# Kernel tuning notes

Hardware: AMD Instinct MI355X
Metric: run time of the kernel (lower is better)

Reference implementation:

```python
import jax, jax.numpy as jnp
import numpy as np

B, S, D, H = 2, 2048, 1024, 16
DEPTH = D // H


def setup_inputs() -> dict:
    key = jax.random.key(0)
    ks = jax.random.split(key, 9)
    sc = 1.0 / np.sqrt(D)
    return {
        "x": jax.random.normal(ks[0], (B, S, D), dtype=jnp.float32),
        "wq": jax.random.normal(ks[1], (D, D), dtype=jnp.float32) * sc,
        "bq": jnp.zeros((D,), dtype=jnp.float32),
        "wk": jax.random.normal(ks[2], (D, D), dtype=jnp.float32) * sc,
        "bk": jnp.zeros((D,), dtype=jnp.float32),
        "wv": jax.random.normal(ks[3], (D, D), dtype=jnp.float32) * sc,
        "bv": jnp.zeros((D,), dtype=jnp.float32),
        "wo": jax.random.normal(ks[4], (D, D), dtype=jnp.float32) * sc,
        "bo": jnp.zeros((D,), dtype=jnp.float32),
    }


def _split_heads(t):
    # [B,S,D] -> [B,H,S,depth]
    return t.reshape(B, S, H, DEPTH).transpose(0, 2, 1, 3)


def reference(x, wq, bq, wk, bk, wv, bv, wo, bo):
    q = _split_heads(x @ wq + bq)
    k = _split_heads(x @ wk + bk)
    v = _split_heads(x @ wv + bv)
    scale = 1.0 / jnp.sqrt(jnp.asarray(DEPTH, dtype=x.dtype))
    logits = jnp.einsum("bhqd,bhkd->bhqk", q, k) * scale
    attn = jax.nn.relu(logits)  # ReLU replaces softmax
    ctx = jnp.einsum("bhqk,bhkd->bhqd", attn, v)
    concat = ctx.transpose(0, 2, 1, 3).reshape(B, S, D)
    out = concat @ wo + bo
    return out, attn
```

## Files before the change

### kernel.cpp

```cpp
#include <hip/hip_runtime.h>
#include <hip/hip_bf16.h>

constexpr int Bn = 2, Sn = 2048, Dn = 1024, Hn = 16, DEP = 64;
constexpr int NTOKn = Bn * Sn;

typedef __bf16 bf16x8 __attribute__((ext_vector_type(8)));
typedef float f32x4 __attribute__((ext_vector_type(4)));

__device__ __forceinline__ unsigned short f2bf(float f) {
    union { __hip_bfloat16 h; unsigned short u; } cv;
    cv.h = __float2bfloat16(f);
    return cv.u;
}

__device__ __forceinline__ void gll16(const void* g, void* l) {
    __builtin_amdgcn_global_load_lds(
        (const __attribute__((address_space(1))) unsigned int*)g,
        (__attribute__((address_space(3))) unsigned int*)l, 16, 0, 0);
}

__global__ __launch_bounds__(256) void k_cvt_x(const float* __restrict__ x,
                                               unsigned short* __restrict__ xb,
                                               int n) {
    int idx = (blockIdx.x * 256 + threadIdx.x) * 4;
    if (idx < n) {
        float4 v = *reinterpret_cast<const float4*>(x + idx);
        ushort4 o;
        o.x = f2bf(v.x); o.y = f2bf(v.y); o.z = f2bf(v.z); o.w = f2bf(v.w);
        *reinterpret_cast<ushort4*>(xb + idx) = o;
    }
}

__global__ __launch_bounds__(256) void k_tconv_w(const float* __restrict__ w0,
                                                 const float* __restrict__ w1,
                                                 const float* __restrict__ w2,
                                                 const float* __restrict__ w3,
                                                 unsigned short* __restrict__ t0,
                                                 unsigned short* __restrict__ t1,
                                                 unsigned short* __restrict__ t2,
                                                 unsigned short* __restrict__ t3) {
    const float* w; unsigned short* tp;
    switch (blockIdx.z) {
        case 0: w = w0; tp = t0; break;
        case 1: w = w1; tp = t1; break;
        case 2: w = w2; tp = t2; break;
        default: w = w3; tp = t3; break;
    }
    __shared__ unsigned short tile[64][65];
    const int k0 = blockIdx.x * 64, n0 = blockIdx.y * 64;
    const int t = threadIdx.x;
    const int c = t & 63, rb = t >> 6;
#pragma unroll
    for (int i = 0; i < 16; ++i) {
        int r = rb + i * 4;
        tile[r][c] = f2bf(w[(size_t)(k0 + r) * Dn + n0 + c]);
    }
    __syncthreads();
#pragma unroll
    for (int i = 0; i < 16; ++i) {
        int n = rb + i * 4;
        tp[(size_t)(n0 + n) * Dn + k0 + c] = tile[c][n];
    }
}

__global__ __launch_bounds__(256) void k_tr_v(const unsigned short* __restrict__ V,
                                              unsigned short* __restrict__ VT) {
    __shared__ unsigned short tile[64][65];
    const int s0 = blockIdx.x * 64;
    const int bh = blockIdx.y;
    const int b = bh >> 4, h = bh & 15;
    const int t = threadIdx.x;
    const int c = t & 63, rb = t >> 6;
#pragma unroll
    for (int i = 0; i < 16; ++i) {
        int r = rb + i * 4;
        tile[r][c] = V[(size_t)(b * Sn + s0 + r) * Dn + h * DEP + c];
    }
    __syncthreads();
#pragma unroll
    for (int i = 0; i < 16; ++i) {
        int d = rb + i * 4;
        VT[(size_t)(bh * DEP + d) * Sn + s0 + c] = tile[c][d];
    }
}

template <bool OUT_F32, bool QKV3>
__global__ __launch_bounds__(256) void k_gemm(const unsigned short* __restrict__ A,
                                              const unsigned short* __restrict__ Bt_,
                                              const float* __restrict__ b0,
                                              const float* __restrict__ b1,
                                              const float* __restrict__ b2,
                                              void* __restrict__ C_,
                                              int M, int N, int K) {
    __shared__ unsigned short As[128][32];
    __shared__ unsigned short Bs[128][32];
    const int t = threadIdx.x;
    const int w = t >> 6, l = t & 63;
    const int m0 = blockIdx.x * 128, n0 = blockIdx.y * 128;
    const int wr = (w >> 1) * 64, wc = (w & 1) * 64;

    const unsigned short* Bt = Bt_;
    const float* bias = b0;
    char* Cb = (char*)C_;
    if (QKV3) {
        const int z = blockIdx.z;
        Bt = Bt_ + (size_t)z * N * K;
        bias = (z == 0) ? b0 : (z == 1 ? b1 : b2);
        Cb = (char*)C_ + (size_t)z * M * N * (OUT_F32 ? 4 : 2);
    }

    const int lrow = t >> 2;
    const int lcol = (t & 3) * 8;
    const unsigned short* gA = A + (size_t)(m0 + lrow) * K + lcol;
    const unsigned short* gB = Bt + (size_t)(n0 + lrow) * K + lcol;
    unsigned short* lA = &As[0][0] + t * 8;
    unsigned short* lB = &Bs[0][0] + t * 8;

    f32x4 acc[4][4] = {};

    for (int k0 = 0; k0 < K; k0 += 32) {
        __syncthreads();
        gll16(gA + k0, lA);
        gll16(gA + (size_t)64 * K + k0, lA + 2048);
        gll16(gB + k0, lB);
        gll16(gB + (size_t)64 * K + k0, lB + 2048);
        __syncthreads();

        bf16x8 af[4], bfv[4];
#pragma unroll
        for (int i = 0; i < 4; ++i)
            af[i] = *reinterpret_cast<const bf16x8*>(&As[wr + i * 16 + (l & 15)][(l >> 4) * 8]);
#pragma unroll
        for (int i = 0; i < 4; ++i)
            bfv[i] = *reinterpret_cast<const bf16x8*>(&Bs[wc + i * 16 + (l & 15)][(l >> 4) * 8]);
#pragma unroll
        for (int mi = 0; mi < 4; ++mi)
#pragma unroll
            for (int ni = 0; ni < 4; ++ni)
                acc[mi][ni] =
                    __builtin_amdgcn_mfma_f32_16x16x32_bf16(af[mi], bfv[ni], acc[mi][ni], 0, 0, 0);
    }

#pragma unroll
    for (int mi = 0; mi < 4; ++mi) {
        const int row = m0 + wr + mi * 16 + (l >> 4) * 4;
#pragma unroll
        for (int ni = 0; ni < 4; ++ni) {
            const int col = n0 + wc + ni * 16 + (l & 15);
            const float bv = bias[col];
#pragma unroll
            for (int i = 0; i < 4; ++i) {
                const float v = acc[mi][ni][i] + bv;
                if (OUT_F32)
                    reinterpret_cast<float*>(Cb)[(size_t)(row + i) * N + col] = v;
                else
                    reinterpret_cast<unsigned short*>(Cb)[(size_t)(row + i) * N + col] = f2bf(v);
            }
        }
    }
}

__global__ __launch_bounds__(256, 2) void k_attn(const unsigned short* __restrict__ Qb,
                                                 const unsigned short* __restrict__ Kb,
                                                 const unsigned short* __restrict__ VTb,
                                                 float* __restrict__ attn,
                                                 unsigned short* __restrict__ ctx) {
    __shared__ unsigned short Ks[128 * 64];
    __shared__ unsigned short Vs[64 * 128];
    __shared__ unsigned short Ps[4][32][136];

    const int t = threadIdx.x;
    const int w = t >> 6, l = t & 63;
    const int q0 = blockIdx.x * 128;
    const int bh = blockIdx.y;
    const int b = bh >> 4, h = bh & 15;
    const float scale = 0.125f;

    bf16x8 qf[2][2];
#pragma unroll
    for (int mi = 0; mi < 2; ++mi)
#pragma unroll
        for (int kk = 0; kk < 2; ++kk)
            qf[mi][kk] = *reinterpret_cast<const bf16x8*>(
                Qb + (size_t)(b * Sn + q0 + w * 32 + mi * 16 + (l & 15)) * Dn + h * DEP +
                kk * 32 + (l >> 4) * 8);

    const int krow = t >> 3;
    const int kcolswz = ((t & 7) * 8) ^ ((krow & 7) << 3);
    const int vrow = t >> 4;
    const int vcolswz = ((t & 15) * 8) ^ ((vrow & 7) << 3);
    unsigned short* lK = Ks + t * 8;
    unsigned short* lV = Vs + t * 8;

    f32x4 ctxa[2][4] = {};
    f32x4 sa[2][8];

    float* const abase = attn + (size_t)bh * Sn * Sn + (size_t)(q0 + w * 32) * Sn;

    auto STAGE = [&](int kb) {
#pragma unroll
        for (int is = 0; is < 4; ++is) {
            gll16(Kb + (size_t)(b * Sn + kb * 128 + is * 32 + krow) * Dn + h * DEP + kcolswz,
                  lK + is * 2048);
            gll16(VTb + (size_t)(bh * DEP + is * 16 + vrow) * Sn + kb * 128 + vcolswz,
                  lV + is * 2048);
        }
    };

    auto QKT = [&]() {
#pragma unroll
        for (int mi = 0; mi < 2; ++mi)
#pragma unroll
            for (int nj = 0; nj < 8; ++nj)
                sa[mi][nj] = (f32x4){0.f, 0.f, 0.f, 0.f};
#pragma unroll
        for (int nj = 0; nj < 8; ++nj) {
            const int kr = nj * 16 + (l & 15);
#pragma unroll
            for (int kk = 0; kk < 2; ++kk) {
                const int kidx = (kr * 64 + kk * 32 + (l >> 4) * 8) ^ ((kr & 7) << 3);
                const bf16x8 bfr = *reinterpret_cast<const bf16x8*>(Ks + kidx);
                sa[0][nj] = __builtin_amdgcn_mfma_f32_16x16x32_bf16(qf[0][kk], bfr, sa[0][nj], 0, 0, 0);
                sa[1][nj] = __builtin_amdgcn_mfma_f32_16x16x32_bf16(qf[1][kk], bfr, sa[1][nj], 0, 0, 0);
            }
        }
#pragma unroll
        for (int mi = 0; mi < 2; ++mi) {
#pragma unroll
            for (int nj = 0; nj < 8; ++nj) {
                f32x4 v = sa[mi][nj];
#pragma unroll
                for (int i = 0; i < 4; ++i) {
                    float p = v[i] * scale;
                    v[i] = p > 0.f ? p : 0.f;
                }
                sa[mi][nj] = v;
                const int kc = nj * 16 + (l & 15);
#pragma unroll
                for (int i = 0; i < 4; ++i)
                    Ps[w][mi * 16 + (l >> 4) * 4 + i][kc] = f2bf(v[i]);
            }
        }
    };

    auto PV = [&]() {
        bf16x8 pf[2][4];
#pragma unroll
        for (int mi = 0; mi < 2; ++mi)
#pragma unroll
            for (int kk = 0; kk < 4; ++kk)
                pf[mi][kk] = *reinterpret_cast<const bf16x8*>(
                    &Ps[w][mi * 16 + (l & 15)][kk * 32 + (l >> 4) * 8]);
#pragma unroll
        for (int nd = 0; nd < 4; ++nd) {
            const int vr = nd * 16 + (l & 15);
#pragma unroll
            for (int kk = 0; kk < 4; ++kk) {
                const int vidx = (vr * 128 + kk * 32 + (l >> 4) * 8) ^ ((vr & 7) << 3);
                const bf16x8 vfr = *reinterpret_cast<const bf16x8*>(Vs + vidx);
                ctxa[0][nd] = __builtin_amdgcn_mfma_f32_16x16x32_bf16(pf[0][kk], vfr, ctxa[0][nd], 0, 0, 0);
                ctxa[1][nd] = __builtin_amdgcn_mfma_f32_16x16x32_bf16(pf[1][kk], vfr, ctxa[1][nd], 0, 0, 0);
            }
        }
    };

    auto STORE_SA = [&](int kb) {
        float* arow = abase + kb * 128;
#pragma unroll
        for (int mi = 0; mi < 2; ++mi)
#pragma unroll
            for (int nj = 0; nj < 8; ++nj) {
                const int kc = nj * 16 + (l & 15);
#pragma unroll
                for (int i = 0; i < 4; ++i)
                    arow[(size_t)(mi * 16 + (l >> 4) * 4 + i) * Sn + kc] = sa[mi][nj][i];
            }
    };

    STAGE(0);
    asm volatile("s_waitcnt vmcnt(0)" ::: "memory");
    __builtin_amdgcn_s_barrier();
    __builtin_amdgcn_sched_barrier(0);
    QKT();
    PV();

    for (int kb = 1; kb < Sn / 128; ++kb) {
        asm volatile("s_waitcnt lgkmcnt(0)" ::: "memory");
        __builtin_amdgcn_s_barrier();
        __builtin_amdgcn_sched_barrier(0);
        STAGE(kb);
        asm volatile("" ::: "memory");
        STORE_SA(kb - 1);
        asm volatile("s_waitcnt vmcnt(63)" ::: "memory");
        __builtin_amdgcn_s_barrier();
        __builtin_amdgcn_sched_barrier(0);
        QKT();
        PV();
    }
    STORE_SA(Sn / 128 - 1);

#pragma unroll
    for (int mi = 0; mi < 2; ++mi) {
#pragma unroll
        for (int nd = 0; nd < 4; ++nd) {
            const int dc = nd * 16 + (l & 15);
#pragma unroll
            for (int i = 0; i < 4; ++i) {
                const int qr = q0 + w * 32 + mi * 16 + (l >> 4) * 4 + i;
                ctx[(size_t)(b * Sn + qr) * Dn + h * DEP + dc] = f2bf(ctxa[mi][nd][i]);
            }
        }
    }
}

extern "C" void kernel_launch(void* const* d_in, const int* in_sizes, int n_in,
                              void* d_out, int out_size, void* d_ws, size_t ws_size,
                              hipStream_t stream) {
    (void)in_sizes; (void)n_in; (void)out_size; (void)ws_size;
    const float* x  = (const float*)d_in[0];
    const float* wq = (const float*)d_in[1];
    const float* bq = (const float*)d_in[2];
    const float* wk = (const float*)d_in[3];
    const float* bk = (const float*)d_in[4];
    const float* wv = (const float*)d_in[5];
    const float* bv = (const float*)d_in[6];
    const float* wo = (const float*)d_in[7];
    const float* bo = (const float*)d_in[8];

    float* out  = (float*)d_out;
    float* attn = out + (size_t)Bn * Sn * Dn;

    char* ws = (char*)d_ws;
    unsigned short* xb = (unsigned short*)ws;  ws += (size_t)NTOKn * Dn * 2;
    unsigned short* wT = (unsigned short*)ws;  ws += (size_t)4 * Dn * Dn * 2;
    unsigned short* qkv = (unsigned short*)ws; ws += (size_t)3 * NTOKn * Dn * 2;
    unsigned short* vT = (unsigned short*)ws;  ws += (size_t)NTOKn * Dn * 2;
    unsigned short* ctx = (unsigned short*)ws;

    const size_t DD = (size_t)Dn * Dn;

    k_cvt_x<<<dim3(NTOKn * Dn / 4 / 256), 256, 0, stream>>>(x, xb, NTOKn * Dn);
    k_tconv_w<<<dim3(16, 16, 4), 256, 0, stream>>>(wq, wk, wv, wo,
                                                   wT, wT + DD, wT + 2 * DD, wT + 3 * DD);
    k_gemm<false, true><<<dim3(32, 8, 3), 256, 0, stream>>>(xb, wT, bq, bk, bv, qkv,
                                                            NTOKn, Dn, Dn);
    k_tr_v<<<dim3(32, 32), 256, 0, stream>>>(qkv + (size_t)2 * NTOKn * Dn, vT);
    k_attn<<<dim3(16, 32), 256, 0, stream>>>(qkv, qkv + (size_t)NTOKn * Dn, vT, attn, ctx);
    k_gemm<true, false><<<dim3(32, 8, 1), 256, 0, stream>>>(ctx, wT + 3 * DD, bo, bo, bo,
                                                            out, NTOKn, Dn, Dn);
}
```

Measured before the change: 224.0 us.

## Replace QKV GEMM with 256x256-tile double-buffered 8-wave pipelined kernel

Adds a dedicated fused QKV projection kernel that uses 256x256 output tiles, 512 threads and 128KB of dynamic LDS. K-tiles are double-buffered with direct global-to-LDS loads issued while MFMAs run, and the LDS layout is swizzled to avoid bank conflicts. Explicit waitcnt, barriers and setprio control the overlap. The goal is to hide load latency and raise reuse over the old 128x128 single-buffered GEMM, at the cost of only 192 blocks and tight hand-scheduled synchronisation.

Result: faster. 215.1 us (-4.0%).

```diff
diff --git a/kernel.cpp b/kernel.cpp
--- a/kernel.cpp
+++ b/kernel.cpp
@@ -84,30 +84,150 @@
     }
 }
 
-template <bool OUT_F32, bool QKV3>
-__global__ __launch_bounds__(256) void k_gemm(const unsigned short* __restrict__ A,
-                                              const unsigned short* __restrict__ Bt_,
-                                              const float* __restrict__ b0,
-                                              const float* __restrict__ b1,
-                                              const float* __restrict__ b2,
-                                              void* __restrict__ C_,
-                                              int M, int N, int K) {
+__global__ __launch_bounds__(512, 2) void k_qkv8(const unsigned short* __restrict__ A,
+                                                 const unsigned short* __restrict__ Bt,
+                                                 const float* __restrict__ bq,
+                                                 const float* __restrict__ bk,
+                                                 const float* __restrict__ bv,
+                                                 unsigned short* __restrict__ qkv) {
+    extern __shared__ char smem[];
+    constexpr int K = 1024, NT = K / 64;
+
+    const int t = threadIdx.x;
+    const int w = t >> 6, l = t & 63;
+    const int wm = w >> 2, wn = w & 3;
+    const int m0 = blockIdx.x * 256;
+    const int n0 = blockIdx.y * 256;
+    const int z = n0 >> 10;
+
+    const float* bias = (z == 0) ? bq : (z == 1 ? bk : bv);
+    float biasv[4];
+#pragma unroll
+    for (int nf = 0; nf < 4; ++nf)
+        biasv[nf] = bias[(n0 + wn * 64 + nf * 16 + (l & 15)) & 1023];
+
+    int aoff[2], boff[2], ldsoff[2];
+#pragma unroll
+    for (int i = 0; i < 2; ++i) {
+        const int idx = i * 512 + t;
+        const int row = idx >> 2;
+        const int s = ((idx & 3) - row - (row >> 2)) & 3;
+        aoff[i] = (m0 + row) * K + s * 8;
+        boff[i] = (n0 + row) * K + s * 8;
+        ldsoff[i] = idx * 16;
+    }
+
+    f32x4 acc[8][4] = {};
+
+#pragma unroll
+    for (int kh = 0; kh < 2; ++kh) {
+        if (kh == 0) {
+#pragma unroll
+            for (int i = 0; i < 2; ++i) gll16(A + aoff[i] + 0 * 64 + 0 * 32, smem + 0 + 0 + ldsoff[i]);
+#pragma unroll
+            for (int i = 0; i < 2; ++i) gll16(Bt + boff[i] + 0 * 64 + 0 * 32, smem + 65536 + 0 + ldsoff[i]);
+        } else {
+#pragma unroll
+            for (int i = 0; i < 2; ++i) gll16(A + aoff[i] + 0 * 64 + 1 * 32, smem + 0 + 16384 + ldsoff[i]);
+#pragma unroll
+            for (int i = 0; i < 2; ++i) gll16(Bt + boff[i] + 0 * 64 + 1 * 32, smem + 65536 + 16384 + ldsoff[i]);
+        }
+    }
+
+    for (int kb = 0; kb < NT; ++kb) {
+        const int c = kb & 1;
+        const int kn = (kb + 1 < NT) ? kb + 1 : NT - 1;
+        const int cn = c ^ 1;
+        const int Abase = c * 32768;
+        const int Bbase = 65536 + c * 32768;
+        const int AbaseN = cn * 32768;
+        const int BbaseN = 65536 + cn * 32768;
+
+        bf16x8 bf[4], af[4];
+
+#pragma unroll
+        for (int ph = 0; ph < 4; ++ph) {
+            const int kk = ph >> 1;
+            const int mb = (ph & 1) * 4;
+
+            if ((ph & 1) == 0) {
+                asm volatile("s_waitcnt vmcnt(4)" ::: "memory");
+            }
+            __builtin_amdgcn_s_barrier();
+            __builtin_amdgcn_sched_barrier(0);
+
+            if ((ph & 1) == 0) {
+#pragma unroll
+                for (int nf = 0; nf < 4; ++nf) {
+                    const int row = wn * 64 + nf * 16 + (l & 15);
+                    const int byte = Bbase + kk * 16384 + row * 64 +
+                                     ((((l >> 4) + row + (row >> 2)) & 3) * 16);
+                    bf[nf] = *reinterpret_cast<const bf16x8*>(smem + byte);
+                }
+            }
+#pragma unroll
+            for (int mfl = 0; mfl < 4; ++mfl) {
+                const int row = wm * 128 + (mb + mfl) * 16 + (l & 15);
+                const int byte = Abase + kk * 16384 + row * 64 +
+                                 ((((l >> 4) + row + (row >> 2)) & 3) * 16);
+                af[mfl] = *reinterpret_cast<const bf16x8*>(smem + byte);
+            }
+
+            {
+                const int khs = ph >> 1;
+                if ((ph & 1) == 0) {
+#pragma unroll
+                    for (int i = 0; i < 2; ++i)
+                        gll16(A + aoff[i] + kn * 64 + khs * 32,
+                              smem + AbaseN + khs * 16384 + ldsoff[i]);
+                } else {
+#pragma unroll
+                    for (int i = 0; i < 2; ++i)
+                        gll16(Bt + boff[i] + kn * 64 + khs * 32,
+                              smem + BbaseN + khs * 16384 + ldsoff[i]);
+                }
+            }
+
+            asm volatile("s_waitcnt lgkmcnt(0)" ::: "memory");
+            __builtin_amdgcn_sched_barrier(0);
+            __builtin_amdgcn_s_setprio(1);
+#pragma unroll
+            for (int mfl = 0; mfl < 4; ++mfl)
+#pragma unroll
+                for (int nf = 0; nf < 4; ++nf)
+                    acc[mb + mfl][nf] = __builtin_amdgcn_mfma_f32_16x16x32_bf16(
+                        af[mfl], bf[nf], acc[mb + mfl][nf], 0, 0, 0);
+            __builtin_amdgcn_s_setprio(0);
+        }
+    }
+
+    asm volatile("s_waitcnt vmcnt(0)" ::: "memory");
+
+    unsigned short* outz = qkv + (size_t)z * NTOKn * Dn;
+#pragma unroll
+    for (int mf = 0; mf < 8; ++mf) {
+        const int row = m0 + wm * 128 + mf * 16 + (l >> 4) * 4;
+#pragma unroll
+        for (int nf = 0; nf < 4; ++nf) {
+            const int col = (n0 + wn * 64 + nf * 16 + (l & 15)) & 1023;
+#pragma unroll
+            for (int i = 0; i < 4; ++i)
+                outz[(size_t)(row + i) * Dn + col] = f2bf(acc[mf][nf][i] + biasv[nf]);
+        }
+    }
+}
+
+__global__ __launch_bounds__(256) void k_gemm_op(const unsigned short* __restrict__ A,
+                                                 const unsigned short* __restrict__ Bt,
+                                                 const float* __restrict__ bias,
+                                                 float* __restrict__ C,
+                                                 int M, int N, int K) {
     __shared__ unsigned short As[128][32];
     __shared__ unsigned short Bs[128][32];
     const int t = threadIdx.x;
     const int w = t >> 6, l = t & 63;
     const int m0 = blockIdx.x * 128, n0 = blockIdx.y * 128;
     const int wr = (w >> 1) * 64, wc = (w & 1) * 64;
-
-    const unsigned short* Bt = Bt_;
-    const float* bias = b0;
-    char* Cb = (char*)C_;
-    if (QKV3) {
-        const int z = blockIdx.z;
-        Bt = Bt_ + (size_t)z * N * K;
-        bias = (z == 0) ? b0 : (z == 1 ? b1 : b2);
-        Cb = (char*)C_ + (size_t)z * M * N * (OUT_F32 ? 4 : 2);
-    }
 
     const int lrow = t >> 2;
     const int lcol = (t & 3) * 8;
@@ -149,13 +269,8 @@
             const int col = n0 + wc + ni * 16 + (l & 15);
             const float bv = bias[col];
 #pragma unroll
-            for (int i = 0; i < 4; ++i) {
-                const float v = acc[mi][ni][i] + bv;
-                if (OUT_F32)
-                    reinterpret_cast<float*>(Cb)[(size_t)(row + i) * N + col] = v;
-                else
-                    reinterpret_cast<unsigned short*>(Cb)[(size_t)(row + i) * N + col] = f2bf(v);
-            }
+            for (int i = 0; i < 4; ++i)
+                C[(size_t)(row + i) * N + col] = acc[mi][ni][i] + bv;
         }
     }
 }
@@ -339,13 +454,18 @@
 
     const size_t DD = (size_t)Dn * Dn;
 
+    static bool attr_set = false;
+    if (!attr_set) {
+        hipFuncSetAttribute(reinterpret_cast<const void*>(k_qkv8),
+                            hipFuncAttributeMaxDynamicSharedMemorySize, 131072);
+        attr_set = true;
+    }
+
     k_cvt_x<<<dim3(NTOKn * Dn / 4 / 256), 256, 0, stream>>>(x, xb, NTOKn * Dn);
     k_tconv_w<<<dim3(16, 16, 4), 256, 0, stream>>>(wq, wk, wv, wo,
                                                    wT, wT + DD, wT + 2 * DD, wT + 3 * DD);
-    k_gemm<false, true><<<dim3(32, 8, 3), 256, 0, stream>>>(xb, wT, bq, bk, bv, qkv,
-                                                            NTOKn, Dn, Dn);
+    k_qkv8<<<dim3(16, 12), 512, 131072, stream>>>(xb, wT, bq, bk, bv, qkv);
     k_tr_v<<<dim3(32, 32), 256, 0, stream>>>(qkv + (size_t)2 * NTOKn * Dn, vT);
     k_attn<<<dim3(16, 32), 256, 0, stream>>>(qkv, qkv + (size_t)NTOKn * Dn, vT, attn, ctx);
-    k_gemm<true, false><<<dim3(32, 8, 1), 256, 0, stream>>>(ctx, wT + 3 * DD, bo, bo, bo,
-                                                            out, NTOKn, Dn, Dn);
-}
+    k_gemm_op<<<dim3(32, 8), 256, 0, stream>>>(ctx, wT + 3 * DD, bo, out, NTOKn, Dn, Dn);
+}
```
